# Kernel tuning notes

Hardware: AMD Instinct MI355X
Metric: run time of the kernel (lower is better)

Reference implementation:

```python
import jax, jax.numpy as jnp
import numpy as np

B = 1024
IN_H, IN_W = 128, 128
KH, KW = 10, 10
SH, SW = 5, 5
PH, PW = 2, 2
HP, WP = IN_H + 2 * PH, IN_W + 2 * PW          # padded dims: 132, 132
NKH = (IN_H - KH + 2 * PH) // SH + 1            # 25
NKW = (IN_W - KW + 2 * PW) // SW + 1            # 25
NK = NKH * NKW                                  # 625


def _build_weight_matrix(kernel_weights):
    """kernel_weights: [NK, KH, KW] -> sparse-structured dense [HP*WP, NK].
    Faithful to LocallyConnected2dV2._create_weight_matrix, vectorized."""
    i = jnp.arange(NK)
    start_i = (i // NKW) * SH                   # [NK]
    start_j = (i % NKW) * SW                    # [NK]
    # flat row index for each (kernel, k, l) tap in padded image
    rows = ((start_i[:, None, None] + jnp.arange(KH)[None, :, None]) * WP
            + start_j[:, None, None] + jnp.arange(KW)[None, None, :])  # [NK,KH,KW]
    rows = rows.reshape(NK, KH * KW)
    cols = i[:, None]                           # [NK,1] broadcasts over taps
    W = jnp.zeros((HP * WP, NK), dtype=kernel_weights.dtype)
    return W.at[rows, cols].set(kernel_weights.reshape(NK, KH * KW))


def setup_inputs() -> dict:
    key = jax.random.key(0)
    kx, kw, kb = jax.random.split(key, 3)
    x = jax.random.normal(kx, (B, IN_H, IN_W), dtype=jnp.float32)
    kernel_weights = jax.random.normal(kw, (NK, KH, KW), dtype=jnp.float32)
    W = _build_weight_matrix(kernel_weights)    # [HP*WP, NK]
    bias = jax.random.normal(kb, (NKH, NKW), dtype=jnp.float32)
    return {"x": x, "W": W, "bias": bias}


def reference(x, W, bias):
    # zero-pad spatial dims, flatten, dense GEMM against sparse-structured W
    xp = jnp.pad(x, ((0, 0), (PH, PH), (PW, PW)))          # [B,HP,WP]
    xf = xp.reshape(x.shape[0], HP * WP)                   # [B,HP*WP]
    out = xf @ W                                           # [B,NK]
    out = out.reshape(x.shape[0], NKH, NKW)
    return out + bias
```

## Files before the change

kernel.cpp:

```cpp
#include <hip/hip_runtime.h>

typedef _Float16 f16x2 __attribute__((ext_vector_type(2)));
typedef __fp16  fp16x2 __attribute__((ext_vector_type(2)));

constexpr int NKW  = 25, NK = 625;
constexpr int WPADR = 132;
constexpr int WPT   = 160;

union U2H { unsigned int u; f16x2 h; fp16x2 p; };

__global__ void gather_wp(const float* __restrict__ W, _Float16* __restrict__ wgp) {
    int t = blockIdx.x * 256 + threadIdx.x;
    if (t >= NK * WPT) return;
    int k = t / WPT, rem = t % WPT;
    int di = rem >> 4, p = rem & 15;
    int ki = k / NKW, kj = k % NKW;
    int o = (5 * kj + 2) & 3;
    int j = p - o;
    float val = 0.f;
    if (j >= 0 && j < 10)
        val = W[(size_t)((ki * 5 + di) * WPADR + kj * 5 + j) * NK + k];
    wgp[t] = (_Float16)val;
}

__device__ __forceinline__ float dot2acc(unsigned int a, unsigned int b, float c) {
    U2H ua, ub; ua.u = a; ub.u = b;
#if __has_builtin(__builtin_amdgcn_fdot2)
    return __builtin_amdgcn_fdot2(ua.h, ub.h, c, false);
#else
    return c + (float)ua.h.x * (float)ub.h.x + (float)ua.h.y * (float)ub.h.y;
#endif
}

template <bool USE_WG>
__global__ __launch_bounds__(256, 4)
void lc2d_img(const float* __restrict__ x, const _Float16* __restrict__ wgp,
              const float* __restrict__ Wfull,
              const float* __restrict__ bias, float* __restrict__ out) {
    __shared__ uint2 xs[70 * 34];

    const int b    = blockIdx.x;
    const int half = blockIdx.y;
    const int P0   = half ? 65 : 0;
    const int NR   = half ? 65 : 70;
    const int K0   = half ? 13 : 0;
    const int NOUT = half ? 300 : 325;
    const int tid  = threadIdx.x;

    for (int i = tid; i < NR * 2; i += 256)
        xs[(i >> 1) * 34 + (i & 1) * 33] = make_uint2(0u, 0u);

    const float* xb = x + ((size_t)b << 14);
    for (int i = tid; i < NR * 32; i += 256) {
        const int idx = i >> 5, q = (i & 31) + 1;
        const int r = P0 + idx - 2;
        uint2 val = make_uint2(0u, 0u);
        if (r >= 0 && r < 128) {
            const float4 v = *reinterpret_cast<const float4*>(xb + (r << 7) + ((q - 1) << 2));
            U2H u0, u1;
            u0.p = __builtin_amdgcn_cvt_pkrtz(v.x, v.y);
            u1.p = __builtin_amdgcn_cvt_pkrtz(v.z, v.w);
            val.x = u0.u; val.y = u1.u;
        }
        xs[idx * 34 + q] = val;
    }
    __syncthreads();

    const uint4* wgp16 = reinterpret_cast<const uint4*>(wgp);

    for (int k_local = tid; k_local < NOUT; k_local += 256) {
        const int k    = K0 * 25 + k_local;
        const int ki_l = k_local / 25;
        const int kj   = k_local - ki_l * 25;
        const uint2* base = xs + ki_l * 5 * 34 + ((5 * kj + 2) >> 2);
        float acc = bias[k];
#pragma unroll
        for (int c = 0; c < 2; ++c) {
            uint4 wq[10];
            if (USE_WG) {
#pragma unroll
                for (int j = 0; j < 10; ++j) wq[j] = wgp16[k * 20 + c * 10 + j];
            } else {
                const int o = (5 * kj + 2) & 3;
#pragma unroll
                for (int j = 0; j < 10; ++j) {
                    const int di = c * 5 + (j >> 1);
                    const int pb = (j & 1) * 8;
                    unsigned int uu[4];
#pragma unroll
                    for (int m = 0; m < 4; ++m) {
                        float f0 = 0.f, f1 = 0.f;
                        const int j0 = pb + 2 * m - o, j1 = pb + 2 * m + 1 - o;
                        const size_t rowb = (size_t)(((K0 + ki_l) * 5 + di) * WPADR + kj * 5);
                        if (j0 >= 0 && j0 < 10) f0 = Wfull[(rowb + j0) * NK + k];
                        if (j1 >= 0 && j1 < 10) f1 = Wfull[(rowb + j1) * NK + k];
                        U2H u; u.p = __builtin_amdgcn_cvt_pkrtz(f0, f1);
                        uu[m] = u.u;
                    }
                    wq[j] = make_uint4(uu[0], uu[1], uu[2], uu[3]);
                }
            }
#pragma unroll
            for (int d2 = 0; d2 < 5; ++d2) {
                const uint2* rowp = base + (c * 5 + d2) * 34;
                const uint2 a0 = rowp[0], a1 = rowp[1], a2 = rowp[2], a3 = rowp[3];
                const uint4 wA = wq[d2 * 2], wB = wq[d2 * 2 + 1];
                acc = dot2acc(a0.x, wA.x, acc);
                acc = dot2acc(a0.y, wA.y, acc);
                acc = dot2acc(a1.x, wA.z, acc);
                acc = dot2acc(a1.y, wA.w, acc);
                acc = dot2acc(a2.x, wB.x, acc);
                acc = dot2acc(a2.y, wB.y, acc);
                acc = dot2acc(a3.x, wB.z, acc);
                acc = dot2acc(a3.y, wB.w, acc);
            }
        }
        out[(size_t)b * NK + k] = acc;
    }
}

extern "C" void kernel_launch(void* const* d_in, const int* in_sizes, int n_in,
                              void* d_out, int out_size, void* d_ws, size_t ws_size,
                              hipStream_t stream) {
    const float* x    = (const float*)d_in[0];
    const float* W    = (const float*)d_in[1];
    const float* bias = (const float*)d_in[2];
    float* out = (float*)d_out;

    const dim3 grid(1024, 2);
    if (ws_size >= (size_t)NK * WPT * sizeof(_Float16)) {
        _Float16* wgp = (_Float16*)d_ws;
        gather_wp<<<(NK * WPT + 255) / 256, 256, 0, stream>>>(W, wgp);
        lc2d_img<true><<<grid, 256, 0, stream>>>(x, wgp, W, bias, out);
    } else {
        lc2d_img<false><<<grid, 256, 0, stream>>>(x, nullptr, W, bias, out);
    }
}
```

Before: 135.4 us.

## Transpose packed weights for coalesced loads, pad LDS rows, split accumulators

The gathered fp16 weight buffer is stored transposed so that adjacent threads (adjacent k) read adjacent 16-byte chunks, making weight loads coalesced. All 20 weight vectors are loaded up front, the LDS row stride goes from 34 to 35 to change the bank mapping, and the dot-product chain is split across two accumulators for more ILP. Launch bounds are relaxed to 2 blocks per SIMD to leave room for the larger register footprint, which may lower occupancy.

```diff
diff --git a/kernel.cpp b/kernel.cpp
--- a/kernel.cpp
+++ b/kernel.cpp
@@ -6,21 +6,22 @@
 constexpr int NKW  = 25, NK = 625;
 constexpr int WPADR = 132;
 constexpr int WPT   = 160;
+constexpr int RST   = 35;
 
 union U2H { unsigned int u; f16x2 h; fp16x2 p; };
 
-__global__ void gather_wp(const float* __restrict__ W, _Float16* __restrict__ wgp) {
+__global__ void gather_wp(const float* __restrict__ W, _Float16* __restrict__ wgpT) {
     int t = blockIdx.x * 256 + threadIdx.x;
     if (t >= NK * WPT) return;
-    int k = t / WPT, rem = t % WPT;
-    int di = rem >> 4, p = rem & 15;
+    int k = t / WPT, p = t % WPT;
+    int di = p >> 4, s = p & 15;
     int ki = k / NKW, kj = k % NKW;
     int o = (5 * kj + 2) & 3;
-    int j = p - o;
+    int j = s - o;
     float val = 0.f;
     if (j >= 0 && j < 10)
         val = W[(size_t)((ki * 5 + di) * WPADR + kj * 5 + j) * NK + k];
-    wgp[t] = (_Float16)val;
+    wgpT[((size_t)(p >> 3) * NK + k) * 8 + (p & 7)] = (_Float16)val;
 }
 
 __device__ __forceinline__ float dot2acc(unsigned int a, unsigned int b, float c) {
@@ -33,11 +34,11 @@
 }
 
 template <bool USE_WG>
-__global__ __launch_bounds__(256, 4)
-void lc2d_img(const float* __restrict__ x, const _Float16* __restrict__ wgp,
+__global__ __launch_bounds__(256, 2)
+void lc2d_img(const float* __restrict__ x, const _Float16* __restrict__ wgpT,
               const float* __restrict__ Wfull,
               const float* __restrict__ bias, float* __restrict__ out) {
-    __shared__ uint2 xs[70 * 34];
+    __shared__ uint2 xs[70 * RST];
 
     const int b    = blockIdx.x;
     const int half = blockIdx.y;
@@ -48,7 +49,7 @@
     const int tid  = threadIdx.x;
 
     for (int i = tid; i < NR * 2; i += 256)
-        xs[(i >> 1) * 34 + (i & 1) * 33] = make_uint2(0u, 0u);
+        xs[(i >> 1) * RST + (i & 1) * 33] = make_uint2(0u, 0u);
 
     const float* xb = x + ((size_t)b << 14);
     for (int i = tid; i < NR * 32; i += 256) {
@@ -62,60 +63,58 @@
             u1.p = __builtin_amdgcn_cvt_pkrtz(v.z, v.w);
             val.x = u0.u; val.y = u1.u;
         }
-        xs[idx * 34 + q] = val;
+        xs[idx * RST + q] = val;
     }
     __syncthreads();
 
-    const uint4* wgp16 = reinterpret_cast<const uint4*>(wgp);
+    const uint4* wt4 = reinterpret_cast<const uint4*>(wgpT);
 
     for (int k_local = tid; k_local < NOUT; k_local += 256) {
-        const int k    = K0 * 25 + k_local;
+        const int k    = K0 * NKW + k_local;
         const int ki_l = k_local / 25;
         const int kj   = k_local - ki_l * 25;
-        const uint2* base = xs + ki_l * 5 * 34 + ((5 * kj + 2) >> 2);
-        float acc = bias[k];
+        const uint2* base = xs + ki_l * 5 * RST + ((5 * kj + 2) >> 2);
+
+        uint4 wq[20];
+        if (USE_WG) {
 #pragma unroll
-        for (int c = 0; c < 2; ++c) {
-            uint4 wq[10];
-            if (USE_WG) {
+            for (int j = 0; j < 20; ++j) wq[j] = wt4[(size_t)j * NK + k];
+        } else {
+            const int o = (5 * kj + 2) & 3;
 #pragma unroll
-                for (int j = 0; j < 10; ++j) wq[j] = wgp16[k * 20 + c * 10 + j];
-            } else {
-                const int o = (5 * kj + 2) & 3;
+            for (int j = 0; j < 20; ++j) {
+                const int di = j >> 1, pb = (j & 1) * 8;
+                unsigned int uu[4];
 #pragma unroll
-                for (int j = 0; j < 10; ++j) {
-                    const int di = c * 5 + (j >> 1);
-                    const int pb = (j & 1) * 8;
-                    unsigned int uu[4];
-#pragma unroll
-                    for (int m = 0; m < 4; ++m) {
-                        float f0 = 0.f, f1 = 0.f;
-                        const int j0 = pb + 2 * m - o, j1 = pb + 2 * m + 1 - o;
-                        const size_t rowb = (size_t)(((K0 + ki_l) * 5 + di) * WPADR + kj * 5);
-                        if (j0 >= 0 && j0 < 10) f0 = Wfull[(rowb + j0) * NK + k];
-                        if (j1 >= 0 && j1 < 10) f1 = Wfull[(rowb + j1) * NK + k];
-                        U2H u; u.p = __builtin_amdgcn_cvt_pkrtz(f0, f1);
-                        uu[m] = u.u;
-                    }
-                    wq[j] = make_uint4(uu[0], uu[1], uu[2], uu[3]);
+                for (int m = 0; m < 4; ++m) {
+                    float f0 = 0.f, f1 = 0.f;
+                    const int j0 = pb + 2 * m - o, j1 = pb + 2 * m + 1 - o;
+                    const size_t rowb = (size_t)(((K0 + ki_l) * 5 + di) * WPADR + kj * 5);
+                    if (j0 >= 0 && j0 < 10) f0 = Wfull[(rowb + j0) * NK + k];
+                    if (j1 >= 0 && j1 < 10) f1 = Wfull[(rowb + j1) * NK + k];
+                    U2H u; u.p = __builtin_amdgcn_cvt_pkrtz(f0, f1);
+                    uu[m] = u.u;
                 }
-            }
-#pragma unroll
-            for (int d2 = 0; d2 < 5; ++d2) {
-                const uint2* rowp = base + (c * 5 + d2) * 34;
-                const uint2 a0 = rowp[0], a1 = rowp[1], a2 = rowp[2], a3 = rowp[3];
-                const uint4 wA = wq[d2 * 2], wB = wq[d2 * 2 + 1];
-                acc = dot2acc(a0.x, wA.x, acc);
-                acc = dot2acc(a0.y, wA.y, acc);
-                acc = dot2acc(a1.x, wA.z, acc);
-                acc = dot2acc(a1.y, wA.w, acc);
-                acc = dot2acc(a2.x, wB.x, acc);
-                acc = dot2acc(a2.y, wB.y, acc);
-                acc = dot2acc(a3.x, wB.z, acc);
-                acc = dot2acc(a3.y, wB.w, acc);
+                wq[j] = make_uint4(uu[0], uu[1], uu[2], uu[3]);
             }
         }
-        out[(size_t)b * NK + k] = acc;
+
+        float acc0 = bias[k], acc1 = 0.f;
+#pragma unroll
+        for (int d = 0; d < 10; ++d) {
+            const uint2* rowp = base + d * RST;
+            const uint2 a0 = rowp[0], a1 = rowp[1], a2 = rowp[2], a3 = rowp[3];
+            const uint4 wA = wq[2 * d], wB = wq[2 * d + 1];
+            acc0 = dot2acc(a0.x, wA.x, acc0);
+            acc1 = dot2acc(a0.y, wA.y, acc1);
+            acc0 = dot2acc(a1.x, wA.z, acc0);
+            acc1 = dot2acc(a1.y, wA.w, acc1);
+            acc0 = dot2acc(a2.x, wB.x, acc0);
+            acc1 = dot2acc(a2.y, wB.y, acc1);
+            acc0 = dot2acc(a3.x, wB.z, acc0);
+            acc1 = dot2acc(a3.y, wB.w, acc1);
+        }
+        out[(size_t)b * NK + k] = acc0 + acc1;
     }
 }
 
@@ -129,9 +128,9 @@
 
     const dim3 grid(1024, 2);
     if (ws_size >= (size_t)NK * WPT * sizeof(_Float16)) {
-        _Float16* wgp = (_Float16*)d_ws;
-        gather_wp<<<(NK * WPT + 255) / 256, 256, 0, stream>>>(W, wgp);
-        lc2d_img<true><<<grid, 256, 0, stream>>>(x, wgp, W, bias, out);
+        _Float16* wgpT = (_Float16*)d_ws;
+        gather_wp<<<(NK * WPT + 255) / 256, 256, 0, stream>>>(W, wgpT);
+        lc2d_img<true><<<grid, 256, 0, stream>>>(x, wgpT, W, bias, out);
     } else {
         lc2d_img<false><<<grid, 256, 0, stream>>>(x, nullptr, W, bias, out);
     }
```

New measurement: 127.8 us. 5.6% less time.
